# Optimization experiments

Hardware: AMD Instinct MI355X
Metric: run time of the kernel (lower is better)

## Reference

```python
import jax, jax.numpy as jnp
import numpy as np

ALPHA, BETA, GAMMA, EPS = 10.0, 0.1, 1.0, 1e-20
MARK_INDEX = jnp.array([0, 29, 88, 117])

B, S, D, P, C, V = 64, 128, 2048, 118, 2, 512


def setup_inputs() -> dict:
    key = jax.random.key(0)
    ks = jax.random.split(key, 9)
    qy_raw = jax.random.uniform(ks[4], (B, S, V), dtype=jnp.float32)
    qy = qy_raw / jnp.sum(qy_raw, axis=-1, keepdims=True)  # probabilities
    return {
        "zs": jax.random.normal(ks[0], (B, S, D), dtype=jnp.float32),
        "rzs": jax.random.normal(ks[1], (B, S, D), dtype=jnp.float32),
        "pts": jax.random.normal(ks[2], (B, S, P, C), dtype=jnp.float32),
        "pts_gt": jax.random.normal(ks[3], (B, S, P, C), dtype=jnp.float32),
        "qy": qy,
        "logits": jax.random.normal(ks[5], (B, S, V), dtype=jnp.float32),
        "best": jax.random.normal(ks[6], (B, P, C), dtype=jnp.float32),
        "best_gt": jax.random.normal(ks[7], (B, P, C), dtype=jnp.float32),
        "mapping": jax.random.randint(ks[8], (B, S), 0, S, dtype=jnp.int64),
        "vector_dims": V,
    }


def _mse(a, b):
    return jnp.mean(jnp.square(a - b))


def reference(zs, rzs, pts, pts_gt, qy, logits, best, best_gt, mapping, vector_dims):
    # KL divergence vs uniform categorical over vector_dims
    log_g = jnp.log(jnp.float32(1.0) / vector_dims)
    kld = jnp.mean(jnp.sum(qy * (jnp.log(qy + EPS) - log_g), axis=-1))

    best_pts_loss = _mse(best, best_gt) + ALPHA * _mse(
        best[..., MARK_INDEX, :], best_gt[..., MARK_INDEX, :]
    )

    # mapping-indexed gather along dim 1 (vectorized form of the double loop;
    # per-element mse means are all over equal-sized slices, so the summed/
    # averaged loop equals a single global mean over the gathered tensors)
    rz_m = jnp.take_along_axis(rzs, mapping[:, :, None], axis=1)          # [B,S,D]
    x_m = jnp.take_along_axis(pts, mapping[:, :, None, None], axis=1)    # [B,S,P,C]
    recon = _mse(rz_m, zs)
    disk = _mse(x_m, pts_gt)
    landmark = _mse(x_m[..., MARK_INDEX, :], pts_gt[..., MARK_INDEX, :])
    pts_loss = disk + ALPHA * landmark

    total = BETA * kld + GAMMA * recon + pts_loss + best_pts_loss
    return total
```

## Files before the change

### kernel.cpp

```cpp
#include <hip/hip_runtime.h>
#include <math.h>

#define NB 64
#define NS 128
#define ND 2048
#define NP 118
#define NC 2
#define NV 512

constexpr int SEG0 = (NB * NS * ND) / 4;
constexpr int SEG1 = (NB * NS * NV) / 4;
constexpr int SEG2 = (NB * NS * NP * NC) / 4;
constexpr int SEG3 = (NB * NP * NC) / 4;
constexpr int TOTAL4 = SEG0 + SEG1 + SEG2 + SEG3;

__global__ __launch_bounds__(256) void cqloss_kernel(
    const float* __restrict__ zs, const float* __restrict__ rzs,
    const float* __restrict__ pts, const float* __restrict__ pts_gt,
    const float* __restrict__ qy,
    const float* __restrict__ best, const float* __restrict__ best_gt,
    const int* __restrict__ mapping, const int* __restrict__ vd,
    float* __restrict__ out)
{
    const float w_recon = 1.0f / 16777216.0f;
    const float w_kld   = 0.1f / 8192.0f;
    const float w_disk  = 1.0f / 1933312.0f;
    const float w_land  = 10.0f / 65536.0f;
    const float w_best  = 1.0f / 15104.0f;
    const float w_bland = 10.0f / 512.0f;
    const float log_g   = -__logf((float)vd[0]);

    float acc = 0.0f;
    int tid = blockIdx.x * blockDim.x + threadIdx.x;
    int stride = gridDim.x * blockDim.x;

    for (int i = tid; i < TOTAL4; i += stride) {
        if (i < SEG0) {
            int base = i << 2;
            int b = base >> 18;
            int rem = base & (262143);
            int s = rem >> 11;
            int d = rem & 2047;
            int m = mapping[(b << 7) + s];
            const float4 z = *(const float4*)(zs + base);
            const float4 r = *(const float4*)(rzs + ((((b << 7) + m) << 11) + d));
            float dx = r.x - z.x, dy = r.y - z.y, dz = r.z - z.z, dw = r.w - z.w;
            acc += w_recon * (dx * dx + dy * dy + dz * dz + dw * dw);
        } else if (i < SEG0 + SEG1) {
            int base = (i - SEG0) << 2;
            const float4 q = *(const float4*)(qy + base);
            acc += w_kld * (q.x * (__logf(q.x + 1e-20f) - log_g)
                          + q.y * (__logf(q.y + 1e-20f) - log_g)
                          + q.z * (__logf(q.z + 1e-20f) - log_g)
                          + q.w * (__logf(q.w + 1e-20f) - log_g));
        } else if (i < SEG0 + SEG1 + SEG2) {
            int k = i - (SEG0 + SEG1);
            int bs = k / 59;
            int qo = k - bs * 59;
            int b = bs >> 7, s = bs & 127;
            int m = mapping[(b << 7) + s];
            int off = qo << 2;
            const float4 x = *(const float4*)(pts + (b * NS + m) * 236 + off);
            const float4 g = *(const float4*)(pts_gt + bs * 236 + off);
            const float* xp = (const float*)&x;
            const float* gp = (const float*)&g;
            #pragma unroll
            for (int j = 0; j < 4; ++j) {
                int p = (off + j) >> 1;
                bool marked = (p == 0) | (p == 29) | (p == 88) | (p == 117);
                float w = w_disk + (marked ? w_land : 0.0f);
                float d = xp[j] - gp[j];
                acc += w * d * d;
            }
        } else {
            int l = i - (SEG0 + SEG1 + SEG2);
            int b = l / 59;
            int qo = l - b * 59;
            int off = qo << 2;
            int base = b * 236 + off;
            const float4 x = *(const float4*)(best + base);
            const float4 g = *(const float4*)(best_gt + base);
            const float* xp = (const float*)&x;
            const float* gp = (const float*)&g;
            #pragma unroll
            for (int j = 0; j < 4; ++j) {
                int p = (off + j) >> 1;
                bool marked = (p == 0) | (p == 29) | (p == 88) | (p == 117);
                float w = w_best + (marked ? w_bland : 0.0f);
                float d = xp[j] - gp[j];
                acc += w * d * d;
            }
        }
    }

    #pragma unroll
    for (int o = 32; o > 0; o >>= 1) acc += __shfl_down(acc, o, 64);

    __shared__ float wsum[4];
    int lane = threadIdx.x & 63;
    int wave = threadIdx.x >> 6;
    if (lane == 0) wsum[wave] = acc;
    __syncthreads();
    if (threadIdx.x == 0) {
        float s = wsum[0] + wsum[1] + wsum[2] + wsum[3];
        atomicAdd(out, s);
    }
}

extern "C" void kernel_launch(void* const* d_in, const int* in_sizes, int n_in,
                              void* d_out, int out_size, void* d_ws, size_t ws_size,
                              hipStream_t stream) {
    const float* zs      = (const float*)d_in[0];
    const float* rzs     = (const float*)d_in[1];
    const float* pts     = (const float*)d_in[2];
    const float* pts_gt  = (const float*)d_in[3];
    const float* qy      = (const float*)d_in[4];
    const float* best    = (const float*)d_in[6];
    const float* best_gt = (const float*)d_in[7];
    const int*   mapping = (const int*)d_in[8];
    const int*   vd      = (const int*)d_in[9];
    float* out = (float*)d_out;

    hipMemsetAsync(out, 0, sizeof(float), stream);

    cqloss_kernel<<<4096, 256, 0, stream>>>(zs, rzs, pts, pts_gt, qy,
                                            best, best_gt, mapping, vd, out);
}
```

Measured before the change: 215.8 us.

## Assign fixed block ranges per loss segment instead of grid-stride loop

```diff
diff --git a/kernel.cpp b/kernel.cpp
--- a/kernel.cpp
+++ b/kernel.cpp
@@ -12,7 +12,12 @@
 constexpr int SEG1 = (NB * NS * NV) / 4;
 constexpr int SEG2 = (NB * NS * NP * NC) / 4;
 constexpr int SEG3 = (NB * NP * NC) / 4;
-constexpr int TOTAL4 = SEG0 + SEG1 + SEG2 + SEG3;
+
+constexpr int RECON_BLOCKS = 4096;
+constexpr int KLD_BLOCKS   = 512;
+constexpr int PTS_BLOCKS   = 512;
+constexpr int BEST_BLOCKS  = 16;
+constexpr int TOTAL_BLOCKS = RECON_BLOCKS + KLD_BLOCKS + PTS_BLOCKS + BEST_BLOCKS;
 
 __global__ __launch_bounds__(256) void cqloss_kernel(
     const float* __restrict__ zs, const float* __restrict__ rzs,
@@ -28,67 +33,129 @@
     const float w_land  = 10.0f / 65536.0f;
     const float w_best  = 1.0f / 15104.0f;
     const float w_bland = 10.0f / 512.0f;
-    const float log_g   = -__logf((float)vd[0]);
 
+    const int t   = threadIdx.x;
+    const int blk = blockIdx.x;
     float acc = 0.0f;
-    int tid = blockIdx.x * blockDim.x + threadIdx.x;
-    int stride = gridDim.x * blockDim.x;
 
-    for (int i = tid; i < TOTAL4; i += stride) {
-        if (i < SEG0) {
-            int base = i << 2;
-            int b = base >> 18;
-            int rem = base & (262143);
-            int s = rem >> 11;
-            int d = rem & 2047;
-            int m = mapping[(b << 7) + s];
-            const float4 z = *(const float4*)(zs + base);
-            const float4 r = *(const float4*)(rzs + ((((b << 7) + m) << 11) + d));
-            float dx = r.x - z.x, dy = r.y - z.y, dz = r.z - z.z, dw = r.w - z.w;
-            acc += w_recon * (dx * dx + dy * dy + dz * dz + dw * dw);
-        } else if (i < SEG0 + SEG1) {
-            int base = (i - SEG0) << 2;
-            const float4 q = *(const float4*)(qy + base);
-            acc += w_kld * (q.x * (__logf(q.x + 1e-20f) - log_g)
-                          + q.y * (__logf(q.y + 1e-20f) - log_g)
-                          + q.z * (__logf(q.z + 1e-20f) - log_g)
-                          + q.w * (__logf(q.w + 1e-20f) - log_g));
-        } else if (i < SEG0 + SEG1 + SEG2) {
-            int k = i - (SEG0 + SEG1);
-            int bs = k / 59;
-            int qo = k - bs * 59;
-            int b = bs >> 7, s = bs & 127;
-            int m = mapping[(b << 7) + s];
-            int off = qo << 2;
-            const float4 x = *(const float4*)(pts + (b * NS + m) * 236 + off);
-            const float4 g = *(const float4*)(pts_gt + bs * 236 + off);
+    __shared__ int mrow[16];
+
+    if (blk < RECON_BLOCKS) {
+        const int row0 = blk << 1;
+        const int m0 = mapping[row0];
+        const int m1 = mapping[row0 + 1];
+        const int b0 = row0 >> 7;
+        const int b1 = (row0 + 1) >> 7;
+        const float4* zp0 = (const float4*)(zs  + ((size_t)row0 << 11));
+        const float4* zp1 = (const float4*)(zs  + ((size_t)(row0 + 1) << 11));
+        const float4* rp0 = (const float4*)(rzs + ((size_t)((b0 << 7) + m0) << 11));
+        const float4* rp1 = (const float4*)(rzs + ((size_t)((b1 << 7) + m1) << 11));
+        float4 za = zp0[t], zb = zp0[t + 256];
+        float4 ra = rp0[t], rb = rp0[t + 256];
+        float4 zc = zp1[t], zd = zp1[t + 256];
+        float4 rc = rp1[t], rd = rp1[t + 256];
+        float s = 0.0f;
+        {
+            float dx = ra.x - za.x, dy = ra.y - za.y, dz = ra.z - za.z, dw = ra.w - za.w;
+            s += dx*dx + dy*dy + dz*dz + dw*dw;
+        }
+        {
+            float dx = rb.x - zb.x, dy = rb.y - zb.y, dz = rb.z - zb.z, dw = rb.w - zb.w;
+            s += dx*dx + dy*dy + dz*dz + dw*dw;
+        }
+        {
+            float dx = rc.x - zc.x, dy = rc.y - zc.y, dz = rc.z - zc.z, dw = rc.w - zc.w;
+            s += dx*dx + dy*dy + dz*dz + dw*dw;
+        }
+        {
+            float dx = rd.x - zd.x, dy = rd.y - zd.y, dz = rd.z - zd.z, dw = rd.w - zd.w;
+            s += dx*dx + dy*dy + dz*dz + dw*dw;
+        }
+        acc = w_recon * s;
+    } else if (blk < RECON_BLOCKS + KLD_BLOCKS) {
+        const int rb = blk - RECON_BLOCKS;
+        const float log_g = -__logf((float)vd[0]);
+        const float4* qp = (const float4*)qy + ((size_t)rb << 11) + t;
+        float4 q[8];
+        #pragma unroll
+        for (int k = 0; k < 8; ++k) q[k] = qp[k * 256];
+        float s = 0.0f;
+        #pragma unroll
+        for (int k = 0; k < 8; ++k) {
+            s += q[k].x * (__logf(q[k].x + 1e-20f) - log_g)
+               + q[k].y * (__logf(q[k].y + 1e-20f) - log_g)
+               + q[k].z * (__logf(q[k].z + 1e-20f) - log_g)
+               + q[k].w * (__logf(q[k].w + 1e-20f) - log_g);
+        }
+        acc = w_kld * s;
+    } else if (blk < RECON_BLOCKS + KLD_BLOCKS + PTS_BLOCKS) {
+        const int rb = blk - (RECON_BLOCKS + KLD_BLOCKS);
+        if (t < 16) mrow[t] = mapping[(rb << 4) + t];
+        __syncthreads();
+        const int bs_base = rb << 4;
+        #pragma unroll
+        for (int j = 0; j < 3; ++j) {
+            const int w = t + j * 256;
+            const unsigned rl = (unsigned)w / 59u;
+            const int qo = w - (int)rl * 59;
+            const int bs = bs_base + (int)rl;
+            const int b  = bs >> 7;
+            const int m  = mrow[rl];
+            const float4 x = *(const float4*)(pts    + ((size_t)((b << 7) + m) * 236 + (qo << 2)));
+            const float4 g = *(const float4*)(pts_gt + ((size_t)(rb * 944 + w) << 2));
             const float* xp = (const float*)&x;
             const float* gp = (const float*)&g;
+            const int p2 = qo << 1;
             #pragma unroll
-            for (int j = 0; j < 4; ++j) {
-                int p = (off + j) >> 1;
-                bool marked = (p == 0) | (p == 29) | (p == 88) | (p == 117);
-                float w = w_disk + (marked ? w_land : 0.0f);
-                float d = xp[j] - gp[j];
-                acc += w * d * d;
+            for (int jj = 0; jj < 4; ++jj) {
+                const int p = p2 + (jj >> 1);
+                const bool marked = (p == 0) | (p == 29) | (p == 88) | (p == 117);
+                const float wgt = w_disk + (marked ? w_land : 0.0f);
+                const float d = xp[jj] - gp[jj];
+                acc += wgt * d * d;
             }
-        } else {
-            int l = i - (SEG0 + SEG1 + SEG2);
-            int b = l / 59;
-            int qo = l - b * 59;
-            int off = qo << 2;
-            int base = b * 236 + off;
-            const float4 x = *(const float4*)(best + base);
-            const float4 g = *(const float4*)(best_gt + base);
+        }
+        {
+            const int w = t + 768;
+            if (w < 944) {
+                const unsigned rl = (unsigned)w / 59u;
+                const int qo = w - (int)rl * 59;
+                const int bs = bs_base + (int)rl;
+                const int b  = bs >> 7;
+                const int m  = mrow[rl];
+                const float4 x = *(const float4*)(pts    + ((size_t)((b << 7) + m) * 236 + (qo << 2)));
+                const float4 g = *(const float4*)(pts_gt + ((size_t)(rb * 944 + w) << 2));
+                const float* xp = (const float*)&x;
+                const float* gp = (const float*)&g;
+                const int p2 = qo << 1;
+                #pragma unroll
+                for (int jj = 0; jj < 4; ++jj) {
+                    const int p = p2 + (jj >> 1);
+                    const bool marked = (p == 0) | (p == 29) | (p == 88) | (p == 117);
+                    const float wgt = w_disk + (marked ? w_land : 0.0f);
+                    const float d = xp[jj] - gp[jj];
+                    acc += wgt * d * d;
+                }
+            }
+        }
+    } else {
+        const int db = blk - (RECON_BLOCKS + KLD_BLOCKS + PTS_BLOCKS);
+        if (t < 236) {
+            const int l = db * 236 + t;
+            const unsigned bq = (unsigned)l / 59u;
+            const int qo = l - (int)bq * 59;
+            const float4 x = *(const float4*)(best    + ((size_t)l << 2));
+            const float4 g = *(const float4*)(best_gt + ((size_t)l << 2));
             const float* xp = (const float*)&x;
             const float* gp = (const float*)&g;
+            const int p2 = qo << 1;
             #pragma unroll
-            for (int j = 0; j < 4; ++j) {
-                int p = (off + j) >> 1;
-                bool marked = (p == 0) | (p == 29) | (p == 88) | (p == 117);
-                float w = w_best + (marked ? w_bland : 0.0f);
-                float d = xp[j] - gp[j];
-                acc += w * d * d;
+            for (int jj = 0; jj < 4; ++jj) {
+                const int p = p2 + (jj >> 1);
+                const bool marked = (p == 0) | (p == 29) | (p == 88) | (p == 117);
+                const float wgt = w_best + (marked ? w_bland : 0.0f);
+                const float d = xp[jj] - gp[jj];
+                acc += wgt * d * d;
             }
         }
     }
@@ -97,13 +164,12 @@
     for (int o = 32; o > 0; o >>= 1) acc += __shfl_down(acc, o, 64);
 
     __shared__ float wsum[4];
-    int lane = threadIdx.x & 63;
-    int wave = threadIdx.x >> 6;
+    const int lane = t & 63;
+    const int wave = t >> 6;
     if (lane == 0) wsum[wave] = acc;
     __syncthreads();
-    if (threadIdx.x == 0) {
-        float s = wsum[0] + wsum[1] + wsum[2] + wsum[3];
-        atomicAdd(out, s);
+    if (t == 0) {
+        atomicAdd(out, wsum[0] + wsum[1] + wsum[2] + wsum[3]);
     }
 }
 
@@ -123,6 +189,6 @@
 
     hipMemsetAsync(out, 0, sizeof(float), stream);
 
-    cqloss_kernel<<<4096, 256, 0, stream>>>(zs, rzs, pts, pts_gt, qy,
-                                            best, best_gt, mapping, vd, out);
+    cqloss_kernel<<<TOTAL_BLOCKS, 256, 0, stream>>>(zs, rzs, pts, pts_gt, qy,
+                                                    best, best_gt, mapping, vd, out);
 }
```

After: 214.9 us. No clear change (-0.4%).
